# Kernel tuning notes

Measured on AMD Instinct MI355X. Metric: run time of the kernel, lower is better.

## Reference

```python
import jax, jax.numpy as jnp
import numpy as np

TEMPERATURE = 8.0  # sqrt(head_dim=64)


def setup_inputs() -> dict:
    key = jax.random.key(0)
    kq, kk, kv, km = jax.random.split(key, 4)
    B, S, D = 16, 2048, 64
    q = jax.random.normal(kq, (B, S, D), dtype=jnp.float32)
    k = jax.random.normal(kk, (B, S, D), dtype=jnp.float32)
    v = jax.random.normal(kv, (B, S, D), dtype=jnp.float32)
    mask = jax.random.randint(km, (B, S, S), 0, 2).astype(jnp.bool_)
    return {"q": q, "k": k, "v": v, "mask": mask}


def reference(q, k, v, mask):
    # latent = q @ k^T / temperature  -> [B, Sq, Sk]
    latent = jnp.einsum('bqd,bkd->bqk', q, k) / TEMPERATURE
    # NOTE: the original fills masked positions with 1e-9 (NOT -inf); keep faithful.
    latent = jnp.where(mask, jnp.float32(1e-9), latent)
    attn = jax.nn.softmax(latent, axis=-1)
    return jnp.einsum('bqk,bkd->bqd', attn, v)
```

## Files before the change

kernel.cpp:

```cpp
#include <hip/hip_runtime.h>
#include <hip/hip_bf16.h>

#define BB 16
#define SS 2048
#define DD 64
#define NT_TILES (SS / 128)
#define TILE_BYTES 16384
#define BUF_BYTES 49152

typedef __attribute__((ext_vector_type(8)))  unsigned short ushort8;
typedef __attribute__((ext_vector_type(8)))  __bf16 bf16x8;
typedef __attribute__((ext_vector_type(16))) float f32x16;
typedef __attribute__((ext_vector_type(4)))  unsigned int uint4v;

static __device__ __forceinline__ unsigned short f2bf(float x) {
    return __builtin_bit_cast(unsigned short, __float2bfloat16(x));
}
static __device__ __forceinline__ unsigned pk2(float a, float b) {
    return (unsigned)f2bf(a) | ((unsigned)f2bf(b) << 16);
}
union F4 { float4 v; float a[4]; };

#define GLDS16(src, dst) __builtin_amdgcn_global_load_lds(                 \
    (const __attribute__((address_space(1))) unsigned int*)(src),          \
    (__attribute__((address_space(3))) unsigned int*)(dst), 16, 0, 0)

__global__ __launch_bounds__(256)
void prepack_kernel(const float* __restrict__ K, const float* __restrict__ V,
                    char* __restrict__ wsK, char* __restrict__ wsV) {
    __shared__ __align__(16) char smem[32768];
    char* Ks = smem;
    char* Vs = smem + 16384;
    const int t  = threadIdx.x;
    const int kt = blockIdx.x;
    const int b  = blockIdx.y;
    const float* Kg = K + (size_t)b * SS * DD;
    const float* Vg = V + (size_t)b * SS * DD;

    #pragma unroll
    for (int j = 0; j < 4; j++) {
        const int idx = 2 * t + 512 * j;
        const int row = idx >> 4;
        const int g   = (idx & 15) >> 1;
        const float* src = Kg + (size_t)(kt * 128) * DD + (size_t)idx * 4;
        F4 fa, fb; fa.v = *(const float4*)src; fb.v = *(const float4*)(src + 4);
        ushort8 u;
        #pragma unroll
        for (int e = 0; e < 4; e++) { u[e] = f2bf(fa.a[e]); u[e + 4] = f2bf(fb.a[e]); }
        *(ushort8*)(Ks + row * 128 + ((g ^ (row & 7)) * 16)) = u;
    }
    {
        const int d0v = (t & 15) * 4;
        const int kkb = (t >> 4) * 4;
        #pragma unroll
        for (int it2 = 0; it2 < 2; it2++) {
            const int kk = kkb + 64 * it2;
            const float* src = Vg + (size_t)(kt * 128 + kk) * DD + d0v;
            F4 r0, r1, r2, r3;
            r0.v = *(const float4*)(src);
            r1.v = *(const float4*)(src + DD);
            r2.v = *(const float4*)(src + 2 * DD);
            r3.v = *(const float4*)(src + 3 * DD);
            #pragma unroll
            for (int e = 0; e < 4; e++) {
                const int d = d0v + e;
                const uint2 wv = make_uint2(pk2(r0.a[e], r1.a[e]), pk2(r2.a[e], r3.a[e]));
                *(uint2*)(Vs + d * 256 + (((kk >> 3) ^ (d & 15)) * 16) + (kk & 7) * 2) = wv;
            }
        }
    }
    __syncthreads();
    char* dK = wsK + (size_t)(b * NT_TILES + kt) * TILE_BYTES;
    char* dV = wsV + (size_t)(b * NT_TILES + kt) * TILE_BYTES;
    #pragma unroll
    for (int j = 0; j < 4; j++) {
        *(float4*)(dK + t * 16 + j * 4096) = *(const float4*)(Ks + t * 16 + j * 4096);
        *(float4*)(dV + t * 16 + j * 4096) = *(const float4*)(Vs + t * 16 + j * 4096);
    }
}

__global__ __launch_bounds__(256, 1)
void sdpa_mfma_kernel(const float* __restrict__ Q, const char* __restrict__ wsK,
                      const char* __restrict__ wsV, const unsigned int* __restrict__ M,
                      float* __restrict__ O) {
    __shared__ __align__(16) char smem[3 * BUF_BYTES];
    char* Qs = smem;
    float* red  = (float*)smem;
    float* denx = (float*)(smem + 24576);

    const int t    = threadIdx.x;
    const int lane = t & 63;
    const int l31  = lane & 31;
    const int half = lane >> 5;
    const int kh   = t >> 6;
    const int b    = blockIdx.y;
    const int q0   = blockIdx.x * 32;

    {
        const int sr = t >> 3, sc = t & 7;
        const float* src = Q + ((size_t)b * SS + q0 + sr) * DD + sc * 8;
        F4 f0, f1; f0.v = *(const float4*)src; f1.v = *(const float4*)(src + 4);
        ushort8 u;
        #pragma unroll
        for (int e = 0; e < 4; e++) {
            u[e]     = f2bf(f0.a[e] * 0.125f);
            u[e + 4] = f2bf(f1.a[e] * 0.125f);
        }
        *(ushort8*)(Qs + sr * 128 + ((sc ^ (sr & 7)) * 16)) = u;
    }
    __syncthreads();

    const int qrow = l31;
    bf16x8 bq[4];
    #pragma unroll
    for (int dc = 0; dc < 4; dc++)
        bq[dc] = __builtin_bit_cast(bf16x8, *(const ushort8*)(
            Qs + qrow * 128 + (((2 * dc + half) ^ (qrow & 7)) * 16)));
    __syncthreads();

    f32x16 On0, On1;
    #pragma unroll
    for (int i = 0; i < 16; i++) { On0[i] = 0.f; On1[i] = 0.f; }
    float den0 = 0.f, den1 = 0.f;

    const char* tKbase = wsK + (size_t)b * NT_TILES * TILE_BYTES;
    const char* tVbase = wsV + (size_t)b * NT_TILES * TILE_BYTES;

    const unsigned int* Msrc = M + (size_t)b * SS * SS
                                 + (size_t)(q0 + (lane >> 3)) * SS
                                 + 32 * kh + 4 * ((lane & 7) ^ (lane >> 3));
    const int voff = ((lane >> 2) * 256)
                   + ((kh ^ ((lane >> 4) & 3)) * 64)
                   + (((lane & 3) ^ ((lane >> 2) & 3)) * 16);
    const int r7 = l31 & 7;

    auto stage = [&](int bufn, int kt) {
        char* wb = smem + bufn * BUF_BYTES + kh * 12288;
        const char* tK = tKbase + (size_t)kt * TILE_BYTES + 32 * kh * 128;
        #pragma unroll
        for (int j = 0; j < 4; j++)
            GLDS16(tK + j * 1024 + lane * 16, wb + j * 1024);
        const char* tV = tVbase + (size_t)kt * TILE_BYTES;
        #pragma unroll
        for (int j = 0; j < 4; j++)
            GLDS16(tV + j * 4096 + voff, wb + 4096 + j * 1024);
        const unsigned int* ms = Msrc + (size_t)kt * 128;
        #pragma unroll
        for (int j = 0; j < 4; j++)
            GLDS16(ms + (size_t)j * 8 * SS, wb + 8192 + j * 1024);
    };

    stage(0, 0);
    stage(1, 1);

    #pragma unroll 1
    for (int kt = 0; kt < NT_TILES; ++kt) {
        const int ktS = (kt + 2 < NT_TILES) ? kt + 2 : NT_TILES - 1;
        stage((kt + 2) % 3, ktS);
        asm volatile("s_waitcnt vmcnt(24)" ::: "memory");
        __builtin_amdgcn_sched_barrier(0);

        const char* wb = smem + (kt % 3) * BUF_BYTES + kh * 12288;

        bf16x8 ak[4];
        #pragma unroll
        for (int dc = 0; dc < 4; dc++)
            ak[dc] = __builtin_bit_cast(bf16x8, *(const ushort8*)(
                wb + l31 * 128 + (((2 * dc + half) ^ r7) * 16)));
        uint4v mt[4];
        #pragma unroll
        for (int g = 0; g < 4; g++)
            mt[g] = *(const uint4v*)(wb + 8192 + l31 * 128 + 16 * ((half + 2 * g) ^ r7));
        bf16x8 av[2][2];
        #pragma unroll
        for (int s2 = 0; s2 < 2; s2++)
            #pragma unroll
            for (int dc = 0; dc < 2; dc++) {
                const int vrow = 32 * dc + l31;
                av[s2][dc] = __builtin_bit_cast(bf16x8, *(const ushort8*)(
                    wb + 4096 + vrow * 64 + (2 * s2 + half) * 16));
            }

        f32x16 S;
        #pragma unroll
        for (int i = 0; i < 16; i++) S[i] = 0.f;
        #pragma unroll
        for (int dc = 0; dc < 4; dc++)
            S = __builtin_amdgcn_mfma_f32_32x32x16_bf16(ak[dc], bq[dc], S, 0, 0, 0);

        float p[16];
        #pragma unroll
        for (int g = 0; g < 4; g++) {
            #pragma unroll
            for (int e = 0; e < 4; e++) {
                const float ev = __expf(S[4 * g + e]);
                const float pv = mt[g][e] ? 1.0f : ev;
                p[4 * g + e] = pv;
                if (g & 1) den1 += pv; else den0 += pv;
            }
        }

        #pragma unroll
        for (int s2 = 0; s2 < 2; s2++) {
            const unsigned o0 = pk2(p[8 * s2 + 0], p[8 * s2 + 1]);
            const unsigned o1 = pk2(p[8 * s2 + 2], p[8 * s2 + 3]);
            const unsigned o2 = pk2(p[8 * s2 + 4], p[8 * s2 + 5]);
            const unsigned o3 = pk2(p[8 * s2 + 6], p[8 * s2 + 7]);
            const unsigned s0 = half ? o0 : o2;
            const unsigned s1 = half ? o1 : o3;
            const unsigned r0 = (unsigned)__shfl_xor((int)s0, 32, 64);
            const unsigned r1 = (unsigned)__shfl_xor((int)s1, 32, 64);
            uint4 bu;
            bu.x = half ? r0 : o0;
            bu.y = half ? r1 : o1;
            bu.z = half ? o2 : r0;
            bu.w = half ? o3 : r1;
            const bf16x8 bp = __builtin_bit_cast(bf16x8, bu);
            On0 = __builtin_amdgcn_mfma_f32_32x32x16_bf16(av[s2][0], bp, On0, 0, 0, 0);
            On1 = __builtin_amdgcn_mfma_f32_32x32x16_bf16(av[s2][1], bp, On1, 0, 0, 0);
        }
    }

    const float den_acc = den0 + den1;
    const float den_tot = den_acc + __shfl_xor(den_acc, 32, 64);

    __syncthreads();
    if (kh != 0) {
        #pragma unroll
        for (int dc = 0; dc < 2; dc++)
            #pragma unroll
            for (int g = 0; g < 4; g++) {
                const f32x16& Oc = dc ? On1 : On0;
                float4 st;
                st.x = Oc[4 * g + 0]; st.y = Oc[4 * g + 1];
                st.z = Oc[4 * g + 2]; st.w = Oc[4 * g + 3];
                *(float4*)((char*)red + (kh - 1) * 8192 + (dc * 4 + g) * 1024 + lane * 16) = st;
            }
        if (lane < 32) denx[kh * 32 + l31] = den_tot;
    }
    __syncthreads();
    if (kh == 0) {
        const float inv = 1.0f / (den_tot + denx[32 + l31] + denx[64 + l31] + denx[96 + l31]);
        float* Og = O + ((size_t)b * SS + q0 + qrow) * DD;
        #pragma unroll
        for (int dc = 0; dc < 2; dc++)
            #pragma unroll
            for (int g = 0; g < 4; g++) {
                const f32x16& Oc = dc ? On1 : On0;
                float4 st;
                st.x = Oc[4 * g + 0]; st.y = Oc[4 * g + 1];
                st.z = Oc[4 * g + 2]; st.w = Oc[4 * g + 3];
                #pragma unroll
                for (int w2 = 0; w2 < 3; w2++) {
                    const float4 pr = *(const float4*)((char*)red + w2 * 8192 +
                                                       (dc * 4 + g) * 1024 + lane * 16);
                    st.x += pr.x; st.y += pr.y; st.z += pr.z; st.w += pr.w;
                }
                st.x *= inv; st.y *= inv; st.z *= inv; st.w *= inv;
                *(float4*)(Og + 32 * dc + 8 * g + 4 * half) = st;
            }
    }
}

extern "C" void kernel_launch(void* const* d_in, const int* in_sizes, int n_in,
                              void* d_out, int out_size, void* d_ws, size_t ws_size,
                              hipStream_t stream) {
    const float* q = (const float*)d_in[0];
    const float* k = (const float*)d_in[1];
    const float* v = (const float*)d_in[2];
    const unsigned int* m = (const unsigned int*)d_in[3];
    float* out = (float*)d_out;

    char* wsK = (char*)d_ws;
    char* wsV = wsK + (size_t)BB * NT_TILES * TILE_BYTES;

    dim3 pgrid(NT_TILES, BB);
    prepack_kernel<<<pgrid, 256, 0, stream>>>(k, v, wsK, wsV);

    dim3 grid(SS / 32, BB);
    sdpa_mfma_kernel<<<grid, 256, 0, stream>>>(q, wsK, wsV, m, out);
}
```

Baseline: 393.8 us.

## Share K/V tiles across two query halves in 512-thread blocks

Each block now covers 64 queries with 8 waves: two groups of four waves share one double-buffered K/V LDS tile. The mask keeps its own triple buffer, split per wave. One wave group loads K and the other loads V, which halves per-query K/V staging traffic and doubles the waves resident per CU, since LDS limited the old kernel to one block per CU. In exchange it adds a workgroup barrier each iteration and uses nearly all of the 160KB of LDS.

```diff
diff --git a/kernel.cpp b/kernel.cpp
--- a/kernel.cpp
+++ b/kernel.cpp
@@ -6,7 +6,8 @@
 #define DD 64
 #define NT_TILES (SS / 128)
 #define TILE_BYTES 16384
-#define BUF_BYTES 49152
+#define KVBUF 32768
+#define MBUF  32768
 
 typedef __attribute__((ext_vector_type(8)))  unsigned short ushort8;
 typedef __attribute__((ext_vector_type(8)))  __bf16 bf16x8;
@@ -79,22 +80,26 @@
     }
 }
 
-__global__ __launch_bounds__(256, 1)
+__global__ __launch_bounds__(512, 1)
 void sdpa_mfma_kernel(const float* __restrict__ Q, const char* __restrict__ wsK,
                       const char* __restrict__ wsV, const unsigned int* __restrict__ M,
                       float* __restrict__ O) {
-    __shared__ __align__(16) char smem[3 * BUF_BYTES];
+    __shared__ __align__(16) char smem[2 * KVBUF + 3 * MBUF];
     char* Qs = smem;
+    char* const Mbase = smem + 2 * KVBUF;
     float* red  = (float*)smem;
-    float* denx = (float*)(smem + 24576);
+    float* denx = (float*)(smem + 49152);
 
     const int t    = threadIdx.x;
     const int lane = t & 63;
     const int l31  = lane & 31;
     const int half = lane >> 5;
-    const int kh   = t >> 6;
+    const int w    = t >> 6;
+    const int kh   = w & 3;
+    const int qs   = w >> 2;
     const int b    = blockIdx.y;
-    const int q0   = blockIdx.x * 32;
+    const int q0   = blockIdx.x * 64;
+    const int q0v  = q0 + 32 * qs;
 
     {
         const int sr = t >> 3, sc = t & 7;
@@ -111,11 +116,12 @@
     __syncthreads();
 
     const int qrow = l31;
+    const int r7   = l31 & 7;
     bf16x8 bq[4];
     #pragma unroll
     for (int dc = 0; dc < 4; dc++)
         bq[dc] = __builtin_bit_cast(bf16x8, *(const ushort8*)(
-            Qs + qrow * 128 + (((2 * dc + half) ^ (qrow & 7)) * 16)));
+            Qs + (32 * qs + qrow) * 128 + (((2 * dc + half) ^ r7) * 16)));
     __syncthreads();
 
     f32x16 On0, On1;
@@ -127,50 +133,60 @@
     const char* tVbase = wsV + (size_t)b * NT_TILES * TILE_BYTES;
 
     const unsigned int* Msrc = M + (size_t)b * SS * SS
-                                 + (size_t)(q0 + (lane >> 3)) * SS
+                                 + (size_t)(q0v + (lane >> 3)) * SS
                                  + 32 * kh + 4 * ((lane & 7) ^ (lane >> 3));
     const int voff = ((lane >> 2) * 256)
                    + ((kh ^ ((lane >> 4) & 3)) * 64)
                    + (((lane & 3) ^ ((lane >> 2) & 3)) * 16);
-    const int r7 = l31 & 7;
-
-    auto stage = [&](int bufn, int kt) {
-        char* wb = smem + bufn * BUF_BYTES + kh * 12288;
-        const char* tK = tKbase + (size_t)kt * TILE_BYTES + 32 * kh * 128;
+
+    auto stage_kv = [&](int bufn, int kt) {
+        char* kvb = smem + bufn * KVBUF;
+        if (qs == 0) {
+            const char* tK = tKbase + (size_t)kt * TILE_BYTES + 32 * kh * 128;
+            #pragma unroll
+            for (int j = 0; j < 4; j++)
+                GLDS16(tK + j * 1024 + lane * 16, kvb + kh * 4096 + j * 1024);
+        } else {
+            const char* tV = tVbase + (size_t)kt * TILE_BYTES;
+            #pragma unroll
+            for (int j = 0; j < 4; j++)
+                GLDS16(tV + j * 4096 + voff, kvb + 16384 + kh * 4096 + j * 1024);
+        }
+    };
+    auto stage_m = [&](int bufn, int kt) {
+        char* mb = Mbase + bufn * MBUF + w * 4096;
+        const unsigned int* ms = Msrc + (size_t)kt * 128;
         #pragma unroll
         for (int j = 0; j < 4; j++)
-            GLDS16(tK + j * 1024 + lane * 16, wb + j * 1024);
-        const char* tV = tVbase + (size_t)kt * TILE_BYTES;
-        #pragma unroll
-        for (int j = 0; j < 4; j++)
-            GLDS16(tV + j * 4096 + voff, wb + 4096 + j * 1024);
-        const unsigned int* ms = Msrc + (size_t)kt * 128;
-        #pragma unroll
-        for (int j = 0; j < 4; j++)
-            GLDS16(ms + (size_t)j * 8 * SS, wb + 8192 + j * 1024);
+            GLDS16(ms + (size_t)j * 8 * SS, mb + j * 1024);
     };
 
-    stage(0, 0);
-    stage(1, 1);
+    stage_kv(0, 0);
+    stage_m(0, 0);
+    stage_m(1, 1);
 
     #pragma unroll 1
     for (int kt = 0; kt < NT_TILES; ++kt) {
-        const int ktS = (kt + 2 < NT_TILES) ? kt + 2 : NT_TILES - 1;
-        stage((kt + 2) % 3, ktS);
-        asm volatile("s_waitcnt vmcnt(24)" ::: "memory");
+        asm volatile("s_waitcnt vmcnt(4)" ::: "memory");
         __builtin_amdgcn_sched_barrier(0);
-
-        const char* wb = smem + (kt % 3) * BUF_BYTES + kh * 12288;
+        __builtin_amdgcn_s_barrier();
+        const int kKV = (kt + 1 < NT_TILES) ? kt + 1 : NT_TILES - 1;
+        const int kM  = (kt + 2 < NT_TILES) ? kt + 2 : NT_TILES - 1;
+        stage_kv((kt + 1) & 1, kKV);
+        stage_m((kt + 2) % 3, kM);
+
+        const char* kvb = smem + (kt & 1) * KVBUF;
+        const char* mb  = Mbase + (kt % 3) * MBUF + w * 4096;
 
         bf16x8 ak[4];
         #pragma unroll
         for (int dc = 0; dc < 4; dc++)
             ak[dc] = __builtin_bit_cast(bf16x8, *(const ushort8*)(
-                wb + l31 * 128 + (((2 * dc + half) ^ r7) * 16)));
+                kvb + kh * 4096 + l31 * 128 + (((2 * dc + half) ^ r7) * 16)));
         uint4v mt[4];
         #pragma unroll
         for (int g = 0; g < 4; g++)
-            mt[g] = *(const uint4v*)(wb + 8192 + l31 * 128 + 16 * ((half + 2 * g) ^ r7));
+            mt[g] = *(const uint4v*)(mb + l31 * 128 + 16 * ((half + 2 * g) ^ r7));
         bf16x8 av[2][2];
         #pragma unroll
         for (int s2 = 0; s2 < 2; s2++)
@@ -178,7 +194,7 @@
             for (int dc = 0; dc < 2; dc++) {
                 const int vrow = 32 * dc + l31;
                 av[s2][dc] = __builtin_bit_cast(bf16x8, *(const ushort8*)(
-                    wb + 4096 + vrow * 64 + (2 * s2 + half) * 16));
+                    kvb + 16384 + kh * 4096 + vrow * 64 + (2 * s2 + half) * 16));
             }
 
         f32x16 S;
@@ -234,14 +250,17 @@
                 float4 st;
                 st.x = Oc[4 * g + 0]; st.y = Oc[4 * g + 1];
                 st.z = Oc[4 * g + 2]; st.w = Oc[4 * g + 3];
-                *(float4*)((char*)red + (kh - 1) * 8192 + (dc * 4 + g) * 1024 + lane * 16) = st;
-            }
-        if (lane < 32) denx[kh * 32 + l31] = den_tot;
+                *(float4*)((char*)red + qs * 24576 + (kh - 1) * 8192 +
+                           (dc * 4 + g) * 1024 + lane * 16) = st;
+            }
+        if (lane < 32) denx[w * 32 + l31] = den_tot;
     }
     __syncthreads();
     if (kh == 0) {
-        const float inv = 1.0f / (den_tot + denx[32 + l31] + denx[64 + l31] + denx[96 + l31]);
-        float* Og = O + ((size_t)b * SS + q0 + qrow) * DD;
+        const float inv = 1.0f / (den_tot + denx[(qs * 4 + 1) * 32 + l31]
+                                          + denx[(qs * 4 + 2) * 32 + l31]
+                                          + denx[(qs * 4 + 3) * 32 + l31]);
+        float* Og = O + ((size_t)b * SS + q0v + qrow) * DD;
         #pragma unroll
         for (int dc = 0; dc < 2; dc++)
             #pragma unroll
@@ -252,8 +271,8 @@
                 st.z = Oc[4 * g + 2]; st.w = Oc[4 * g + 3];
                 #pragma unroll
                 for (int w2 = 0; w2 < 3; w2++) {
-                    const float4 pr = *(const float4*)((char*)red + w2 * 8192 +
-                                                       (dc * 4 + g) * 1024 + lane * 16);
+                    const float4 pr = *(const float4*)((char*)red + qs * 24576 +
+                                        w2 * 8192 + (dc * 4 + g) * 1024 + lane * 16);
                     st.x += pr.x; st.y += pr.y; st.z += pr.z; st.w += pr.w;
                 }
                 st.x *= inv; st.y *= inv; st.z *= inv; st.w *= inv;
@@ -277,6 +296,6 @@
     dim3 pgrid(NT_TILES, BB);
     prepack_kernel<<<pgrid, 256, 0, stream>>>(k, v, wsK, wsV);
 
-    dim3 grid(SS / 32, BB);
-    sdpa_mfma_kernel<<<grid, 256, 0, stream>>>(q, wsK, wsV, m, out);
-}
+    dim3 grid(SS / 64, BB);
+    sdpa_mfma_kernel<<<grid, 512, 0, stream>>>(q, wsK, wsV, m, out);
+}
```

Result: faster. 382.1 us (-3.0%).
